# Performance work log

Hardware: AMD Instinct MI355X
Metric: run time of the kernel (lower is better)

Reference implementation:

```python
import jax, jax.numpy as jnp
import numpy as np

NTYPES = 2
NATOMS = (512, 512)
N = 1024          # total atoms
NN = 128          # neighbors per type
M = NTYPES * NN   # 256 neighbor slots per atom
D = 25            # last embedding width
FH = 240          # fitting hidden width
B = 8
RMIN, RMAX = 5.8, 6.0


def _embed_mlp(s, W0, b0, W1, b1, W2, b2):
    # DeepMD-style resnet embedding net: 1 -> D -> D -> D, tanh + skip
    h = jnp.tanh(s @ W0 + b0)
    h = h + jnp.tanh(h @ W1 + b1)
    h = h + jnp.tanh(h @ W2 + b2)
    return h


def setup_inputs() -> dict:
    key = jax.random.key(0)
    ks = jax.random.split(key, 20)
    # relative positions; components in [-4.5, 4.5] so |r| spans <5.8, [5.8,6.0), >=6.0
    image_dR = (jax.random.uniform(ks[0], (B, N, NTYPES, NN, 3), jnp.float32) - 0.5) * 9.0
    # 0 == empty neighbor slot (mask = list_neigh > 0); index-1 in [0, N)
    list_neigh = jax.random.randint(ks[1], (B, N, NTYPES, NN), 0, 1025)
    davg = 0.1 * jax.random.normal(ks[2], (NTYPES, M, 4), jnp.float32)
    dstd = jax.random.uniform(ks[3], (NTYPES, M, 4), jnp.float32, 0.5, 1.5)
    P = NTYPES * NTYPES
    eW0 = jax.random.normal(ks[4], (P, 1, D), jnp.float32)
    eb0 = 0.1 * jax.random.normal(ks[5], (P, D), jnp.float32)
    eW1 = jax.random.normal(ks[6], (P, D, D), jnp.float32) / np.sqrt(D)
    eb1 = 0.1 * jax.random.normal(ks[7], (P, D), jnp.float32)
    eW2 = jax.random.normal(ks[8], (P, D, D), jnp.float32) / np.sqrt(D)
    eb2 = 0.1 * jax.random.normal(ks[9], (P, D), jnp.float32)
    fW0 = jax.random.normal(ks[10], (NTYPES, 16 * D, FH), jnp.float32) / np.sqrt(16 * D)
    fb0 = 0.1 * jax.random.normal(ks[11], (NTYPES, FH), jnp.float32)
    fW1 = jax.random.normal(ks[12], (NTYPES, FH, FH), jnp.float32) / np.sqrt(FH)
    fb1 = 0.1 * jax.random.normal(ks[13], (NTYPES, FH), jnp.float32)
    fW2 = jax.random.normal(ks[14], (NTYPES, FH, FH), jnp.float32) / np.sqrt(FH)
    fb2 = 0.1 * jax.random.normal(ks[15], (NTYPES, FH), jnp.float32)
    fW3 = jax.random.normal(ks[16], (NTYPES, FH, 1), jnp.float32) / np.sqrt(FH)
    fb3 = 0.1 * jax.random.normal(ks[17], (NTYPES, 1), jnp.float32)
    ener_shift = 0.01 * jax.random.normal(ks[18], (NTYPES,), jnp.float32)
    return {
        'image_dR': image_dR, 'list_neigh': list_neigh,
        'davg': davg, 'dstd': dstd,
        'eW0': eW0, 'eb0': eb0, 'eW1': eW1, 'eb1': eb1, 'eW2': eW2, 'eb2': eb2,
        'fW0': fW0, 'fb0': fb0, 'fW1': fW1, 'fb1': fb1, 'fW2': fW2, 'fb2': fb2,
        'fW3': fW3, 'fb3': fb3, 'ener_shift': ener_shift,
        'dfeat': jnp.zeros((1,), jnp.float32),
        'Egroup_weight': jnp.zeros((1,), jnp.float32),
        'divider': jnp.ones((1,), jnp.float32),
    }


def _forward(image_dR, list_neigh, davg, dstd,
             eW0, eb0, eW1, eb1, eW2, eb2,
             fW0, fb0, fW1, fb1, fW2, fb2, fW3, fb3, ener_shift):
    dR = image_dR.reshape(B, N, M, 3)
    neigh = list_neigh.reshape(B, N, M)
    mask = neigh > 0
    mf = mask.astype(dR.dtype)
    dR2 = jnp.sum(dR * dR, axis=-1)                       # [B,N,M]
    safe_dR2 = jnp.where(mask, dR2, 1.0)
    Rij = jnp.sqrt(safe_dR2)
    inr = mf / Rij                                        # 1/|r|, 0 off-mask
    x = Rij * mf                                          # nr = dR2/Rij = |r|
    Ri_xyz = dR / safe_dR2[..., None] * mf[..., None]     # r / |r|^2
    inr2 = inr * inr
    inr4 = inr2 * inr2
    inr3 = inr4 * x
    # smooth switching function on [RMIN, RMAX]
    u = (x - RMIN) / (RMAX - RMIN)
    poly = u * u * u * (-6.0 * u * u + 15.0 * u - 10.0) + 1.0
    dpoly = (3.0 * u * u * (-6.0 * u * u + 15.0 * u - 10.0)
             + u * u * u * (-12.0 * u + 15.0)) / (RMAX - RMIN)
    mid = (x >= RMIN) & (x < RMAX)
    vv = jnp.where(x < RMIN, 1.0, jnp.where(mid, poly, 0.0)) * mf
    dvv = jnp.where(mid, dpoly, 0.0) * mf
    Ri_pre = jnp.concatenate([inr[..., None], Ri_xyz], axis=-1)   # [B,N,M,4]
    common = (dvv * inr)[..., None] * dR                          # [B,N,M,3]
    row0 = dR * (inr3 * vv)[..., None] - Ri_pre[..., 0:1] * common
    eye = jnp.eye(3, dtype=dR.dtype)
    outer = (2.0 * dR[..., :, None] * dR[..., None, :] * inr4[..., None, None]
             - eye * inr2[..., None, None])                       # [B,N,M,3,3]
    rows = outer * vv[..., None, None] - Ri_pre[..., 1:4, None] * common[..., None, :]
    Ri_d = jnp.concatenate([row0[..., None, :], rows], axis=-2) * mf[..., None, None]  # [B,N,M,4,3]
    Ri = Ri_pre * vv[..., None]
    # per-type normalization stats broadcast over atoms of each type
    davg_res = jnp.concatenate([jnp.broadcast_to(davg[t], (NATOMS[t], M, 4)) for t in range(NTYPES)], axis=0)
    dstd_res = jnp.concatenate([jnp.broadcast_to(dstd[t], (NATOMS[t], M, 4)) for t in range(NTYPES)], axis=0)
    Ri = (Ri - davg_res) / dstd_res
    Ri_d = Ri_d / dstd_res[..., None]

    def ei_fn(Ri_n):
        Ei_list = []
        start = 0
        for t in range(NTYPES):
            na = NATOMS[t]
            Rt = jax.lax.slice_in_dim(Ri_n, start, start + na, axis=1)  # [B,na,M,4]
            acc = jnp.zeros((B, na, 4, D), Ri_n.dtype)
            for t1 in range(NTYPES):
                p = t * NTYPES + t1
                blk = Rt[:, :, t1 * NN:(t1 + 1) * NN]                  # [B,na,NN,4]
                G = _embed_mlp(blk[..., 0:1], eW0[p], eb0[p], eW1[p], eb1[p], eW2[p], eb2[p])
                acc = acc + jnp.einsum('bnkd,bnke->bnde', blk, G)
            acc = acc * (4.0 / (NN * NTYPES * 4))
            DRt = jnp.einsum('bnde,bndf->bnef', acc, acc[..., :16]).reshape(B, na, D * 16)
            h = jnp.tanh(DRt @ fW0[t] + fb0[t])
            h = h + jnp.tanh(h @ fW1[t] + fb1[t])
            h = h + jnp.tanh(h @ fW2[t] + fb2[t])
            Ei_list.append(h @ fW3[t] + fb3[t] + ener_shift[t])
            start += na
        return jnp.concatenate(Ei_list, axis=1)   # [B,N,1]

    Ei, vjpf = jax.vjp(ei_fn, Ri)
    dE, = vjpf(jnp.ones_like(Ei))                 # dEi/dRi  [B,N,M,4]
    Etot = jnp.sum(Ei, axis=1)                    # [B,1]
    pair = jnp.einsum('bnmd,bnmdx->bnmx', dE, Ri_d)   # per-pair force term [B,N,M,3]
    F_self = -jnp.sum(pair, axis=2)
    j = neigh - 1
    valid = j >= 0
    flat_idx = jnp.where(valid, j, N) + jnp.arange(B)[:, None, None] * (N + 1)
    contrib = jnp.where(valid[..., None], pair, 0.0)
    seg = jax.ops.segment_sum(contrib.reshape(-1, 3), flat_idx.reshape(-1), num_segments=B * (N + 1))
    F = F_self + seg.reshape(B, N + 1, 3)[:, :N]
    return Etot, Ei, F


def reference(image_dR, list_neigh, davg, dstd,
              eW0, eb0, eW1, eb1, eW2, eb2,
              fW0, fb0, fW1, fb1, fW2, fb2, fW3, fb3, ener_shift,
              dfeat, Egroup_weight, divider):
    # dfeat / Egroup_weight / divider are in the torch forward signature but unused
    return _forward(image_dR, list_neigh, davg, dstd,
                    eW0, eb0, eW1, eb1, eW2, eb2,
                    fW0, fb0, fW1, fb1, fW2, fb2, fW3, fb3, ener_shift)
```

## Files before the change

### kernel.cpp

```cpp
#include <hip/hip_runtime.h>

#define DEV __device__ __forceinline__

namespace {

constexpr int B_ = 8;
constexpr int N_ = 1024;
constexpr int M_ = 256;
constexpr int D_ = 25;
constexpr int FH_ = 240;
constexpr int NATOM = B_ * N_;
constexpr float CSC = 1.0f / 256.0f;

DEV float fast_tanh(float x) {
  float ax = fabsf(x);
  float e = __expf(-2.0f * ax);
  float r = (1.0f - e) * __builtin_amdgcn_rcpf(1.0f + e);
  return copysignf(r, x);
}

template <bool WANT_RID>
DEV void compute_geom(float dx, float dy, float dz, int nb, int t, int m,
                      const float* __restrict__ davg, const float* __restrict__ dstd,
                      float* __restrict__ blk, float* __restrict__ rid) {
  float mf = (nb > 0) ? 1.0f : 0.0f;
  float dr2 = dx * dx + dy * dy + dz * dz;
  float safe = (nb > 0) ? dr2 : 1.0f;
  float rs = __builtin_amdgcn_rsqf(safe);
  float rij = safe * rs;
  float inr = mf * rs;
  float x = rij * mf;
  float inr2 = inr * inr;
  float inr4 = inr2 * inr2;
  float inr3 = inr4 * x;
  float u = (x - 5.8f) * 5.0f;
  float uu = u * u;
  float A = -6.0f * uu + 15.0f * u - 10.0f;
  float poly = uu * u * A + 1.0f;
  float dpoly = (3.0f * uu * A + uu * u * (-12.0f * u + 15.0f)) * 5.0f;
  bool mid = (x >= 5.8f) && (x < 6.0f);
  float vv = ((x < 5.8f) ? 1.0f : (mid ? poly : 0.0f)) * mf;
  float dvv = (mid ? dpoly : 0.0f) * mf;
  float pre[4];
  pre[0] = inr;
  pre[1] = dx * inr2;
  pre[2] = dy * inr2;
  pre[3] = dz * inr2;
  int bidx = (t * M_ + m) * 4;
  float4 av = *(const float4*)(davg + bidx);
  float4 sv = *(const float4*)(dstd + bidx);
  float avf[4] = {av.x, av.y, av.z, av.w};
  float rsv[4] = {__builtin_amdgcn_rcpf(sv.x), __builtin_amdgcn_rcpf(sv.y),
                  __builtin_amdgcn_rcpf(sv.z), __builtin_amdgcn_rcpf(sv.w)};
#pragma unroll
  for (int d = 0; d < 4; ++d) blk[d] = (pre[d] * vv - avf[d]) * rsv[d];
  if (WANT_RID) {
    float dv[3] = {dx, dy, dz};
    float ci = dvv * inr;
    float com[3];
#pragma unroll
    for (int c = 0; c < 3; ++c) com[c] = ci * dv[c];
    float iv = inr3 * vv;
#pragma unroll
    for (int c = 0; c < 3; ++c)
      rid[c] = (dv[c] * iv - pre[0] * com[c]) * mf * rsv[0];
#pragma unroll
    for (int r = 0; r < 3; ++r) {
#pragma unroll
      for (int c = 0; c < 3; ++c) {
        float outer = 2.0f * dv[r] * dv[c] * inr4 - ((r == c) ? inr2 : 0.0f);
        rid[(1 + r) * 3 + c] = (outer * vv - pre[1 + r] * com[c]) * mf * rsv[1 + r];
      }
    }
  }
}

DEV void embed_fwd(float s, const float* __restrict__ W0, const float* __restrict__ b0,
                   const float* __restrict__ W1, const float* __restrict__ b1,
                   const float* __restrict__ W2, const float* __restrict__ b2,
                   float* __restrict__ h0, float* __restrict__ t1v,
                   float* __restrict__ h1, float* __restrict__ t2v) {
#pragma unroll
  for (int e = 0; e < D_; ++e) h0[e] = fast_tanh(fmaf(s, W0[e], b0[e]));
  float a[D_];
#pragma unroll
  for (int e = 0; e < D_; ++e) a[e] = b1[e];
#pragma unroll
  for (int f = 0; f < D_; ++f) {
    float hf = h0[f];
#pragma unroll
    for (int e = 0; e < D_; ++e) a[e] = fmaf(hf, W1[f * D_ + e], a[e]);
  }
#pragma unroll
  for (int e = 0; e < D_; ++e) { t1v[e] = fast_tanh(a[e]); h1[e] = h0[e] + t1v[e]; }
#pragma unroll
  for (int e = 0; e < D_; ++e) a[e] = b2[e];
#pragma unroll
  for (int f = 0; f < D_; ++f) {
    float hf = h1[f];
#pragma unroll
    for (int e = 0; e < D_; ++e) a[e] = fmaf(hf, W2[f * D_ + e], a[e]);
  }
#pragma unroll
  for (int e = 0; e < D_; ++e) t2v[e] = fast_tanh(a[e]);
}

__global__ __launch_bounds__(256, 2) void k_embed_acc(
    const float* __restrict__ dR, const int* __restrict__ neigh,
    const float* __restrict__ davg, const float* __restrict__ dstd,
    const float* __restrict__ eW0, const float* __restrict__ eb0,
    const float* __restrict__ eW1, const float* __restrict__ eb1,
    const float* __restrict__ eW2, const float* __restrict__ eb2,
    float* __restrict__ acc_ws) {
  __shared__ float sG[M_ * D_];
  __shared__ float4 sBlk[M_];
  int atom = blockIdx.x;
  int n = atom & (N_ - 1);
  int t = (n >= 512) ? 1 : 0;
  int m = threadIdx.x;
  int p = __builtin_amdgcn_readfirstlane(t * 2 + (m >> 7));
  const float* W0 = eW0 + p * D_;
  const float* b0 = eb0 + p * D_;
  const float* W1 = eW1 + p * D_ * D_;
  const float* b1 = eb1 + p * D_;
  const float* W2 = eW2 + p * D_ * D_;
  const float* b2 = eb2 + p * D_;
  int base = atom * M_ + m;
  float dx = dR[base * 3 + 0];
  float dy = dR[base * 3 + 1];
  float dz = dR[base * 3 + 2];
  int nb = neigh[base];
  float blk[4];
  compute_geom<false>(dx, dy, dz, nb, t, m, davg, dstd, blk, nullptr);
  float h0[D_], t1v[D_], h1[D_], t2v[D_];
  embed_fwd(blk[0], W0, b0, W1, b1, W2, b2, h0, t1v, h1, t2v);
#pragma unroll
  for (int e = 0; e < D_; ++e) sG[m * D_ + e] = h1[e] + t2v[e];
  sBlk[m] = make_float4(blk[0], blk[1], blk[2], blk[3]);
  __syncthreads();
  if (threadIdx.x < 100) {
    int d = threadIdx.x & 3;
    int e = threadIdx.x >> 2;
    const float* sb = (const float*)sBlk;
    float sum = 0.0f;
    for (int mm = 0; mm < M_; ++mm)
      sum = fmaf(sb[mm * 4 + d], sG[mm * D_ + e], sum);
    acc_ws[atom * 100 + d * D_ + e] = sum * CSC;
  }
}

__global__ __launch_bounds__(256) void k_fit(
    const float* __restrict__ acc_ws,
    const float* __restrict__ fW0, const float* __restrict__ fb0,
    const float* __restrict__ fW1, const float* __restrict__ fb1,
    const float* __restrict__ fW2, const float* __restrict__ fb2,
    const float* __restrict__ fW3, const float* __restrict__ fb3,
    const float* __restrict__ ener_shift,
    float* __restrict__ dacc_ws, float* __restrict__ out) {
  constexpr int AB = 8;
  __shared__ float sAcc[AB][100];
  __shared__ float sX[AB][400];
  __shared__ float sH0[AB][FH_];
  __shared__ float sT1[AB][FH_];
  __shared__ float sH1[AB][FH_];
  __shared__ float sT2[AB][FH_];
  __shared__ float sEi[AB];
  int a0 = blockIdx.x * AB;
  int bb = a0 >> 10;
  int n0 = a0 & (N_ - 1);
  int t = (n0 >= 512) ? 1 : 0;
  int tid = threadIdx.x;
  for (int idx = tid; idx < AB * 100; idx += 256)
    ((float*)sAcc)[idx] = acc_ws[a0 * 100 + idx];
  if (tid < AB) sEi[tid] = 0.0f;
  __syncthreads();
  for (int idx = tid; idx < AB * 400; idx += 256) {
    int a = idx / 400; int r = idx % 400; int e = r >> 4; int f = r & 15;
    const float* A = sAcc[a];
    sX[a][r] = A[e] * A[f] + A[25 + e] * A[25 + f] + A[50 + e] * A[50 + f] +
               A[75 + e] * A[75 + f];
  }
  __syncthreads();
  const float* W0 = fW0 + t * 400 * FH_;
  const float* W1 = fW1 + t * FH_ * FH_;
  const float* W2 = fW2 + t * FH_ * FH_;
  const float* B0 = fb0 + t * FH_;
  const float* B1 = fb1 + t * FH_;
  const float* B2 = fb2 + t * FH_;
  const float* W3 = fW3 + t * FH_;
  int j = tid;
  if (j < FH_) {
    float acc8[AB];
#pragma unroll
    for (int a = 0; a < AB; ++a) acc8[a] = B0[j];
    for (int i = 0; i < 400; ++i) {
      float w = W0[i * FH_ + j];
#pragma unroll
      for (int a = 0; a < AB; ++a) acc8[a] = fmaf(sX[a][i], w, acc8[a]);
    }
#pragma unroll
    for (int a = 0; a < AB; ++a) sH0[a][j] = fast_tanh(acc8[a]);
  }
  __syncthreads();
  if (j < FH_) {
    float acc8[AB];
#pragma unroll
    for (int a = 0; a < AB; ++a) acc8[a] = B1[j];
    for (int f = 0; f < FH_; ++f) {
      float w = W1[f * FH_ + j];
#pragma unroll
      for (int a = 0; a < AB; ++a) acc8[a] = fmaf(sH0[a][f], w, acc8[a]);
    }
#pragma unroll
    for (int a = 0; a < AB; ++a) {
      float tv = fast_tanh(acc8[a]);
      sT1[a][j] = tv;
      sH1[a][j] = sH0[a][j] + tv;
    }
  }
  __syncthreads();
  if (j < FH_) {
    float acc8[AB];
#pragma unroll
    for (int a = 0; a < AB; ++a) acc8[a] = B2[j];
    for (int f = 0; f < FH_; ++f) {
      float w = W2[f * FH_ + j];
#pragma unroll
      for (int a = 0; a < AB; ++a) acc8[a] = fmaf(sH1[a][f], w, acc8[a]);
    }
    float w3 = W3[j];
#pragma unroll
    for (int a = 0; a < AB; ++a) {
      float tv = fast_tanh(acc8[a]);
      sT2[a][j] = tv;
      atomicAdd(&sEi[a], (sH1[a][j] + tv) * w3);
    }
  }
  __syncthreads();
  if (tid < AB) {
    float ei = sEi[tid] + fb3[t] + ener_shift[t];
    out[8 + a0 + tid] = ei;
    atomicAdd(&out[bb], ei);
  }
  if (j < FH_) {
    float w3 = W3[j];
#pragma unroll
    for (int a = 0; a < AB; ++a) {
      float tv = sT2[a][j];
      sT2[a][j] = w3 * (1.0f - tv * tv);
    }
  }
  __syncthreads();
  if (j < FH_) {
    float w3 = W3[j];
    float acc8[AB];
#pragma unroll
    for (int a = 0; a < AB; ++a) acc8[a] = w3;
    for (int k = 0; k < FH_; ++k) {
      float w = W2[j * FH_ + k];
#pragma unroll
      for (int a = 0; a < AB; ++a) acc8[a] = fmaf(sT2[a][k], w, acc8[a]);
    }
#pragma unroll
    for (int a = 0; a < AB; ++a) {
      float dh1 = acc8[a];
      float tv = sT1[a][j];
      sH1[a][j] = dh1;
      sT1[a][j] = dh1 * (1.0f - tv * tv);
    }
  }
  __syncthreads();
  if (j < FH_) {
    float acc8[AB];
#pragma unroll
    for (int a = 0; a < AB; ++a) acc8[a] = sH1[a][j];
    for (int k = 0; k < FH_; ++k) {
      float w = W1[j * FH_ + k];
#pragma unroll
      for (int a = 0; a < AB; ++a) acc8[a] = fmaf(sT1[a][k], w, acc8[a]);
    }
#pragma unroll
    for (int a = 0; a < AB; ++a) {
      float h0v = sH0[a][j];
      sH0[a][j] = acc8[a] * (1.0f - h0v * h0v);
    }
  }
  __syncthreads();
  for (int i = tid; i < 400; i += 256) {
    float acc8[AB];
#pragma unroll
    for (int a = 0; a < AB; ++a) acc8[a] = 0.0f;
    for (int jj = 0; jj < FH_; ++jj) {
      float w = W0[i * FH_ + jj];
#pragma unroll
      for (int a = 0; a < AB; ++a) acc8[a] = fmaf(sH0[a][jj], w, acc8[a]);
    }
#pragma unroll
    for (int a = 0; a < AB; ++a) sX[a][i] = acc8[a];
  }
  __syncthreads();
  for (int idx = tid; idx < AB * 100; idx += 256) {
    int a = idx / 100; int r = idx % 100; int d = r / 25; int e = r % 25;
    const float* A = sAcc[a];
    const float* DX = sX[a];
    float sum = 0.0f;
#pragma unroll
    for (int f = 0; f < 16; ++f) sum = fmaf(DX[e * 16 + f], A[d * 25 + f], sum);
    if (e < 16) {
#pragma unroll
      for (int e2 = 0; e2 < 25; ++e2) sum = fmaf(DX[e2 * 16 + e], A[d * 25 + e2], sum);
    }
    dacc_ws[a0 * 100 + idx] = sum;
  }
}

__global__ __launch_bounds__(256, 2) void k_bwd_force(
    const float* __restrict__ dR, const int* __restrict__ neigh,
    const float* __restrict__ davg, const float* __restrict__ dstd,
    const float* __restrict__ eW0, const float* __restrict__ eb0,
    const float* __restrict__ eW1, const float* __restrict__ eb1,
    const float* __restrict__ eW2, const float* __restrict__ eb2,
    const float* __restrict__ dacc_ws, float* __restrict__ out) {
  __shared__ float sF[3];
  int atom = blockIdx.x;
  int bb = atom >> 10;
  int n = atom & (N_ - 1);
  int t = (n >= 512) ? 1 : 0;
  int m = threadIdx.x;
  if (m < 3) sF[m] = 0.0f;
  __syncthreads();
  int p = __builtin_amdgcn_readfirstlane(t * 2 + (m >> 7));
  const float* W0 = eW0 + p * D_;
  const float* b0 = eb0 + p * D_;
  const float* W1 = eW1 + p * D_ * D_;
  const float* b1 = eb1 + p * D_;
  const float* W2 = eW2 + p * D_ * D_;
  const float* b2 = eb2 + p * D_;
  const float* dac = dacc_ws + atom * 100;
  int base = atom * M_ + m;
  float dx = dR[base * 3 + 0];
  float dy = dR[base * 3 + 1];
  float dz = dR[base * 3 + 2];
  int nb = neigh[base];
  float blk[4], rid[12];
  compute_geom<true>(dx, dy, dz, nb, t, m, davg, dstd, blk, rid);
  float h0[D_], t1v[D_], h1[D_], t2v[D_];
  embed_fwd(blk[0], W0, b0, W1, b1, W2, b2, h0, t1v, h1, t2v);
  float dblk[4];
#pragma unroll
  for (int d = 0; d < 4; ++d) {
    float s = 0.0f;
#pragma unroll
    for (int e = 0; e < D_; ++e) s = fmaf(dac[d * D_ + e], h1[e] + t2v[e], s);
    dblk[d] = s * CSC;
  }
  float dG[D_];
#pragma unroll
  for (int e = 0; e < D_; ++e)
    dG[e] = CSC * (dac[e] * blk[0] + dac[25 + e] * blk[1] +
                   dac[50 + e] * blk[2] + dac[75 + e] * blk[3]);
  float g[D_];
#pragma unroll
  for (int e = 0; e < D_; ++e) g[e] = dG[e] * (1.0f - t2v[e] * t2v[e]);
#pragma unroll
  for (int e = 0; e < D_; ++e) {
    float s = dG[e];
#pragma unroll
    for (int f = 0; f < D_; ++f) s = fmaf(g[f], W2[e * D_ + f], s);
    dG[e] = s;
  }
#pragma unroll
  for (int e = 0; e < D_; ++e) g[e] = dG[e] * (1.0f - t1v[e] * t1v[e]);
#pragma unroll
  for (int e = 0; e < D_; ++e) {
    float s = dG[e];
#pragma unroll
    for (int f = 0; f < D_; ++f) s = fmaf(g[f], W1[e * D_ + f], s);
    dG[e] = s;
  }
  float ds = 0.0f;
#pragma unroll
  for (int e = 0; e < D_; ++e) ds = fmaf(dG[e] * (1.0f - h0[e] * h0[e]), W0[e], ds);
  float dE0 = dblk[0] + ds, dE1 = dblk[1], dE2 = dblk[2], dE3 = dblk[3];
  float px = dE0 * rid[0] + dE1 * rid[3] + dE2 * rid[6] + dE3 * rid[9];
  float py = dE0 * rid[1] + dE1 * rid[4] + dE2 * rid[7] + dE3 * rid[10];
  float pz = dE0 * rid[2] + dE1 * rid[5] + dE2 * rid[8] + dE3 * rid[11];
  atomicAdd(&sF[0], px);
  atomicAdd(&sF[1], py);
  atomicAdd(&sF[2], pz);
  if (nb > 0) {
    int jn = nb - 1;
    int fi = 8 + NATOM + (bb * N_ + jn) * 3;
    atomicAdd(&out[fi + 0], px);
    atomicAdd(&out[fi + 1], py);
    atomicAdd(&out[fi + 2], pz);
  }
  __syncthreads();
  if (m < 3) atomicAdd(&out[8 + NATOM + atom * 3 + m], -sF[m]);
}

}

extern "C" void kernel_launch(void* const* d_in, const int* in_sizes, int n_in,
                              void* d_out, int out_size, void* d_ws, size_t ws_size,
                              hipStream_t stream) {
  (void)in_sizes; (void)n_in; (void)ws_size;
  const float* image_dR   = (const float*)d_in[0];
  const int*   list_neigh = (const int*)d_in[1];
  const float* davg       = (const float*)d_in[2];
  const float* dstd       = (const float*)d_in[3];
  const float* eW0        = (const float*)d_in[4];
  const float* eb0        = (const float*)d_in[5];
  const float* eW1        = (const float*)d_in[6];
  const float* eb1        = (const float*)d_in[7];
  const float* eW2        = (const float*)d_in[8];
  const float* eb2        = (const float*)d_in[9];
  const float* fW0        = (const float*)d_in[10];
  const float* fb0        = (const float*)d_in[11];
  const float* fW1        = (const float*)d_in[12];
  const float* fb1        = (const float*)d_in[13];
  const float* fW2        = (const float*)d_in[14];
  const float* fb2        = (const float*)d_in[15];
  const float* fW3        = (const float*)d_in[16];
  const float* fb3        = (const float*)d_in[17];
  const float* ener_shift = (const float*)d_in[18];
  float* out = (float*)d_out;
  float* acc_ws  = (float*)d_ws;
  float* dacc_ws = acc_ws + NATOM * 100;

  hipMemsetAsync(d_out, 0, (size_t)out_size * sizeof(float), stream);
  k_embed_acc<<<NATOM, 256, 0, stream>>>(image_dR, list_neigh, davg, dstd,
                                         eW0, eb0, eW1, eb1, eW2, eb2, acc_ws);
  k_fit<<<NATOM / 8, 256, 0, stream>>>(acc_ws, fW0, fb0, fW1, fb1, fW2, fb2,
                                       fW3, fb3, ener_shift, dacc_ws, out);
  k_bwd_force<<<NATOM, 256, 0, stream>>>(image_dR, list_neigh, davg, dstd,
                                         eW0, eb0, eW1, eb1, eW2, eb2,
                                         dacc_ws, out);
}
```

Before: 1.054 ms.

## Hand-unroll embedding nets into scalars and restructure reductions across all kernels

Replaces the array-based embedding forward and backward code with macro-expanded scalar variables so everything stays in registers. Raises k_embed_acc and k_fit occupancy hints to 4 blocks per SM and transposes the shared G/blk tiles so the contraction reads float4 vectors. The backward kernel splits geometry into a block pass and a force pass that folds dE into the rid terms directly, and it reduces per-atom self forces with wave shuffles before the shared atomics. k_fit now sums the per-atom energies in shared memory before issuing one global atomic. Higher occupancy hints may force register spills.

```diff
diff --git a/kernel.cpp b/kernel.cpp
--- a/kernel.cpp
+++ b/kernel.cpp
@@ -1,6 +1,13 @@
 #include <hip/hip_runtime.h>
 
 #define DEV __device__ __forceinline__
+
+#define RA(F) F(0) F(1) F(2) F(3) F(4) F(5) F(6) F(7) F(8) F(9) F(10) F(11) \
+  F(12) F(13) F(14) F(15) F(16) F(17) F(18) F(19) F(20) F(21) F(22) F(23) F(24)
+#define RB(F,j) F(j,0) F(j,1) F(j,2) F(j,3) F(j,4) F(j,5) F(j,6) F(j,7) F(j,8) \
+  F(j,9) F(j,10) F(j,11) F(j,12) F(j,13) F(j,14) F(j,15) F(j,16) F(j,17) \
+  F(j,18) F(j,19) F(j,20) F(j,21) F(j,22) F(j,23) F(j,24)
+#define AP8(F) F(0) F(1) F(2) F(3) F(4) F(5) F(6) F(7)
 
 namespace {
 
@@ -19,10 +26,36 @@
   return copysignf(r, x);
 }
 
-template <bool WANT_RID>
-DEV void compute_geom(float dx, float dy, float dz, int nb, int t, int m,
-                      const float* __restrict__ davg, const float* __restrict__ dstd,
-                      float* __restrict__ blk, float* __restrict__ rid) {
+DEV void geom_blk(float dx, float dy, float dz, int nb, int t, int m,
+                  const float* __restrict__ davg, const float* __restrict__ dstd,
+                  float& o0, float& o1, float& o2, float& o3) {
+  float mf = (nb > 0) ? 1.0f : 0.0f;
+  float dr2 = dx * dx + dy * dy + dz * dz;
+  float safe = (nb > 0) ? dr2 : 1.0f;
+  float rs = __builtin_amdgcn_rsqf(safe);
+  float rij = safe * rs;
+  float inr = mf * rs;
+  float x = rij * mf;
+  float inr2 = inr * inr;
+  float u = (x - 5.8f) * 5.0f;
+  float uu = u * u;
+  float A = -6.0f * uu + 15.0f * u - 10.0f;
+  float poly = uu * u * A + 1.0f;
+  bool mid = (x >= 5.8f) && (x < 6.0f);
+  float vv = ((x < 5.8f) ? 1.0f : (mid ? poly : 0.0f)) * mf;
+  int bidx = (t * M_ + m) * 4;
+  float4 av = *(const float4*)(davg + bidx);
+  float4 sv = *(const float4*)(dstd + bidx);
+  o0 = (inr * vv - av.x) * __builtin_amdgcn_rcpf(sv.x);
+  o1 = (dx * inr2 * vv - av.y) * __builtin_amdgcn_rcpf(sv.y);
+  o2 = (dy * inr2 * vv - av.z) * __builtin_amdgcn_rcpf(sv.z);
+  o3 = (dz * inr2 * vv - av.w) * __builtin_amdgcn_rcpf(sv.w);
+}
+
+DEV void geom_force(float dx, float dy, float dz, int nb, int t, int m,
+                    const float* __restrict__ dstd,
+                    float dE0, float dE1, float dE2, float dE3,
+                    float& px, float& py, float& pz) {
   float mf = (nb > 0) ? 1.0f : 0.0f;
   float dr2 = dx * dx + dy * dy + dz * dz;
   float safe = (nb > 0) ? dr2 : 1.0f;
@@ -41,115 +74,108 @@
   bool mid = (x >= 5.8f) && (x < 6.0f);
   float vv = ((x < 5.8f) ? 1.0f : (mid ? poly : 0.0f)) * mf;
   float dvv = (mid ? dpoly : 0.0f) * mf;
-  float pre[4];
-  pre[0] = inr;
-  pre[1] = dx * inr2;
-  pre[2] = dy * inr2;
-  pre[3] = dz * inr2;
   int bidx = (t * M_ + m) * 4;
-  float4 av = *(const float4*)(davg + bidx);
   float4 sv = *(const float4*)(dstd + bidx);
-  float avf[4] = {av.x, av.y, av.z, av.w};
-  float rsv[4] = {__builtin_amdgcn_rcpf(sv.x), __builtin_amdgcn_rcpf(sv.y),
-                  __builtin_amdgcn_rcpf(sv.z), __builtin_amdgcn_rcpf(sv.w)};
-#pragma unroll
-  for (int d = 0; d < 4; ++d) blk[d] = (pre[d] * vv - avf[d]) * rsv[d];
-  if (WANT_RID) {
-    float dv[3] = {dx, dy, dz};
-    float ci = dvv * inr;
-    float com[3];
-#pragma unroll
-    for (int c = 0; c < 3; ++c) com[c] = ci * dv[c];
-    float iv = inr3 * vv;
-#pragma unroll
-    for (int c = 0; c < 3; ++c)
-      rid[c] = (dv[c] * iv - pre[0] * com[c]) * mf * rsv[0];
-#pragma unroll
-    for (int r = 0; r < 3; ++r) {
-#pragma unroll
-      for (int c = 0; c < 3; ++c) {
-        float outer = 2.0f * dv[r] * dv[c] * inr4 - ((r == c) ? inr2 : 0.0f);
-        rid[(1 + r) * 3 + c] = (outer * vv - pre[1 + r] * com[c]) * mf * rsv[1 + r];
-      }
-    }
-  }
-}
-
-DEV void embed_fwd(float s, const float* __restrict__ W0, const float* __restrict__ b0,
-                   const float* __restrict__ W1, const float* __restrict__ b1,
-                   const float* __restrict__ W2, const float* __restrict__ b2,
-                   float* __restrict__ h0, float* __restrict__ t1v,
-                   float* __restrict__ h1, float* __restrict__ t2v) {
-#pragma unroll
-  for (int e = 0; e < D_; ++e) h0[e] = fast_tanh(fmaf(s, W0[e], b0[e]));
-  float a[D_];
-#pragma unroll
-  for (int e = 0; e < D_; ++e) a[e] = b1[e];
-#pragma unroll
-  for (int f = 0; f < D_; ++f) {
-    float hf = h0[f];
-#pragma unroll
-    for (int e = 0; e < D_; ++e) a[e] = fmaf(hf, W1[f * D_ + e], a[e]);
-  }
-#pragma unroll
-  for (int e = 0; e < D_; ++e) { t1v[e] = fast_tanh(a[e]); h1[e] = h0[e] + t1v[e]; }
-#pragma unroll
-  for (int e = 0; e < D_; ++e) a[e] = b2[e];
-#pragma unroll
-  for (int f = 0; f < D_; ++f) {
-    float hf = h1[f];
-#pragma unroll
-    for (int e = 0; e < D_; ++e) a[e] = fmaf(hf, W2[f * D_ + e], a[e]);
-  }
-#pragma unroll
-  for (int e = 0; e < D_; ++e) t2v[e] = fast_tanh(a[e]);
-}
-
-__global__ __launch_bounds__(256, 2) void k_embed_acc(
+  float e0 = dE0 * mf * __builtin_amdgcn_rcpf(sv.x);
+  float e1 = dE1 * mf * __builtin_amdgcn_rcpf(sv.y);
+  float e2 = dE2 * mf * __builtin_amdgcn_rcpf(sv.z);
+  float e3 = dE3 * mf * __builtin_amdgcn_rcpf(sv.w);
+  float ci = dvv * inr;
+  float comx = ci * dx, comy = ci * dy, comz = ci * dz;
+  float iv = inr3 * vv;
+  float pre0 = inr, pre1 = dx * inr2, pre2 = dy * inr2, pre3 = dz * inr2;
+  float txx = 2.0f * dx * dx * inr4 - inr2;
+  float tyy = 2.0f * dy * dy * inr4 - inr2;
+  float tzz = 2.0f * dz * dz * inr4 - inr2;
+  float txy = 2.0f * dx * dy * inr4;
+  float txz = 2.0f * dx * dz * inr4;
+  float tyz = 2.0f * dy * dz * inr4;
+  px = e0 * (dx * iv - pre0 * comx) + e1 * (txx * vv - pre1 * comx) +
+       e2 * (txy * vv - pre2 * comx) + e3 * (txz * vv - pre3 * comx);
+  py = e0 * (dy * iv - pre0 * comy) + e1 * (txy * vv - pre1 * comy) +
+       e2 * (tyy * vv - pre2 * comy) + e3 * (tyz * vv - pre3 * comy);
+  pz = e0 * (dz * iv - pre0 * comz) + e1 * (txz * vv - pre1 * comz) +
+       e2 * (tyz * vv - pre2 * comz) + e3 * (tzz * vv - pre3 * comz);
+}
+
+#define K1H0(e) float h##e = fast_tanh(fmaf(s0, W0p[e], b0p[e]));
+#define K1A1(e) float a##e = b1p[e];
+#define K1M1E(f,e) a##e = fmaf(hf, W1p[(f)*25+(e)], a##e);
+#define K1M1R(f) { const float hf = h##f; RB(K1M1E, f) }
+#define K1H1(e) h##e += fast_tanh(a##e);
+#define K1A2(e) a##e = b2p[e];
+#define K1M2E(f,e) a##e = fmaf(hf, W2p[(f)*25+(e)], a##e);
+#define K1M2R(f) { const float hf = h##f; RB(K1M2E, f) }
+#define K1ST(e) sGT[e][m] = h##e + fast_tanh(a##e);
+
+__global__ __launch_bounds__(256, 4) void k_embed_acc(
     const float* __restrict__ dR, const int* __restrict__ neigh,
     const float* __restrict__ davg, const float* __restrict__ dstd,
     const float* __restrict__ eW0, const float* __restrict__ eb0,
     const float* __restrict__ eW1, const float* __restrict__ eb1,
     const float* __restrict__ eW2, const float* __restrict__ eb2,
     float* __restrict__ acc_ws) {
-  __shared__ float sG[M_ * D_];
-  __shared__ float4 sBlk[M_];
+  __shared__ float sGT[D_][260];
+  __shared__ float sBT[4][260];
   int atom = blockIdx.x;
   int n = atom & (N_ - 1);
   int t = (n >= 512) ? 1 : 0;
   int m = threadIdx.x;
   int p = __builtin_amdgcn_readfirstlane(t * 2 + (m >> 7));
-  const float* W0 = eW0 + p * D_;
-  const float* b0 = eb0 + p * D_;
-  const float* W1 = eW1 + p * D_ * D_;
-  const float* b1 = eb1 + p * D_;
-  const float* W2 = eW2 + p * D_ * D_;
-  const float* b2 = eb2 + p * D_;
+  const float* W0p = eW0 + p * D_;
+  const float* b0p = eb0 + p * D_;
+  const float* W1p = eW1 + p * 625;
+  const float* b1p = eb1 + p * D_;
+  const float* W2p = eW2 + p * 625;
+  const float* b2p = eb2 + p * D_;
   int base = atom * M_ + m;
   float dx = dR[base * 3 + 0];
   float dy = dR[base * 3 + 1];
   float dz = dR[base * 3 + 2];
   int nb = neigh[base];
-  float blk[4];
-  compute_geom<false>(dx, dy, dz, nb, t, m, davg, dstd, blk, nullptr);
-  float h0[D_], t1v[D_], h1[D_], t2v[D_];
-  embed_fwd(blk[0], W0, b0, W1, b1, W2, b2, h0, t1v, h1, t2v);
-#pragma unroll
-  for (int e = 0; e < D_; ++e) sG[m * D_ + e] = h1[e] + t2v[e];
-  sBlk[m] = make_float4(blk[0], blk[1], blk[2], blk[3]);
+  float bb0, bb1, bb2, bb3;
+  geom_blk(dx, dy, dz, nb, t, m, davg, dstd, bb0, bb1, bb2, bb3);
+  float s0 = bb0;
+  RA(K1H0)
+  RA(K1A1)
+  RA(K1M1R)
+  RA(K1H1)
+  RA(K1A2)
+  RA(K1M2R)
+  RA(K1ST)
+  sBT[0][m] = bb0; sBT[1][m] = bb1; sBT[2][m] = bb2; sBT[3][m] = bb3;
   __syncthreads();
   if (threadIdx.x < 100) {
+    int e = threadIdx.x >> 2;
     int d = threadIdx.x & 3;
-    int e = threadIdx.x >> 2;
-    const float* sb = (const float*)sBlk;
+    const float4* g4 = (const float4*)(&sGT[e][0]);
+    const float4* b4 = (const float4*)(&sBT[d][0]);
     float sum = 0.0f;
-    for (int mm = 0; mm < M_; ++mm)
-      sum = fmaf(sb[mm * 4 + d], sG[mm * D_ + e], sum);
+    for (int k = 0; k < 64; ++k) {
+      float4 g = g4[k];
+      float4 b = b4[k];
+      sum += b.x * g.x + b.y * g.y + b.z * g.z + b.w * g.w;
+    }
     acc_ws[atom * 100 + d * D_ + e] = sum * CSC;
   }
 }
 
-__global__ __launch_bounds__(256) void k_fit(
+#define DECL8(v) float c0=(v),c1=(v),c2=(v),c3=(v),c4=(v),c5=(v),c6=(v),c7=(v);
+#define F8X(q)  c##q = fmaf(sX[q][i], w, c##q);
+#define F8H0(q) c##q = fmaf(sH0[q][f], w, c##q);
+#define F8H1(q) c##q = fmaf(sH1[q][f], w, c##q);
+#define F8T2(q) c##q = fmaf(sT2[q][k], w, c##q);
+#define F8T1(q) c##q = fmaf(sT1[q][k], w, c##q);
+#define F8G0(q) c##q = fmaf(sH0[q][jj], w, c##q);
+#define L0S(q) sH0[q][j] = fast_tanh(c##q);
+#define L1S(q) { float tv = fast_tanh(c##q); sT1[q][j] = tv; sH1[q][j] = sH0[q][j] + tv; }
+#define L2S(q) { float tv = fast_tanh(c##q); sT2[q][j] = tv; atomicAdd(&sEi[q], (sH1[q][j] + tv) * w3); }
+#define G2S(q) { float tv = sT2[q][j]; sT2[q][j] = w3 * (1.0f - tv * tv); }
+#define D1S(q) { float dh1 = c##q; float tv = sT1[q][j]; sH1[q][j] = dh1; sT1[q][j] = dh1 * (1.0f - tv * tv); }
+#define D0S(q) { float h0v = sH0[q][j]; sH0[q][j] = c##q * (1.0f - h0v * h0v); }
+#define DXS(q) sX[q][i] = c##q;
+
+__global__ __launch_bounds__(256, 4) void k_fit(
     const float* __restrict__ acc_ws,
     const float* __restrict__ fW0, const float* __restrict__ fb0,
     const float* __restrict__ fW1, const float* __restrict__ fb1,
@@ -190,113 +216,56 @@
   const float* W3 = fW3 + t * FH_;
   int j = tid;
   if (j < FH_) {
-    float acc8[AB];
-#pragma unroll
-    for (int a = 0; a < AB; ++a) acc8[a] = B0[j];
-    for (int i = 0; i < 400; ++i) {
-      float w = W0[i * FH_ + j];
-#pragma unroll
-      for (int a = 0; a < AB; ++a) acc8[a] = fmaf(sX[a][i], w, acc8[a]);
-    }
-#pragma unroll
-    for (int a = 0; a < AB; ++a) sH0[a][j] = fast_tanh(acc8[a]);
-  }
-  __syncthreads();
-  if (j < FH_) {
-    float acc8[AB];
-#pragma unroll
-    for (int a = 0; a < AB; ++a) acc8[a] = B1[j];
-    for (int f = 0; f < FH_; ++f) {
-      float w = W1[f * FH_ + j];
-#pragma unroll
-      for (int a = 0; a < AB; ++a) acc8[a] = fmaf(sH0[a][f], w, acc8[a]);
-    }
-#pragma unroll
-    for (int a = 0; a < AB; ++a) {
-      float tv = fast_tanh(acc8[a]);
-      sT1[a][j] = tv;
-      sH1[a][j] = sH0[a][j] + tv;
-    }
-  }
-  __syncthreads();
-  if (j < FH_) {
-    float acc8[AB];
-#pragma unroll
-    for (int a = 0; a < AB; ++a) acc8[a] = B2[j];
-    for (int f = 0; f < FH_; ++f) {
-      float w = W2[f * FH_ + j];
-#pragma unroll
-      for (int a = 0; a < AB; ++a) acc8[a] = fmaf(sH1[a][f], w, acc8[a]);
-    }
+    DECL8(B0[j])
+    for (int i = 0; i < 400; ++i) { float w = W0[i * FH_ + j]; AP8(F8X) }
+    AP8(L0S)
+  }
+  __syncthreads();
+  if (j < FH_) {
+    DECL8(B1[j])
+    for (int f = 0; f < FH_; ++f) { float w = W1[f * FH_ + j]; AP8(F8H0) }
+    AP8(L1S)
+  }
+  __syncthreads();
+  if (j < FH_) {
+    DECL8(B2[j])
+    for (int f = 0; f < FH_; ++f) { float w = W2[f * FH_ + j]; AP8(F8H1) }
     float w3 = W3[j];
-#pragma unroll
-    for (int a = 0; a < AB; ++a) {
-      float tv = fast_tanh(acc8[a]);
-      sT2[a][j] = tv;
-      atomicAdd(&sEi[a], (sH1[a][j] + tv) * w3);
-    }
+    AP8(L2S)
   }
   __syncthreads();
   if (tid < AB) {
     float ei = sEi[tid] + fb3[t] + ener_shift[t];
     out[8 + a0 + tid] = ei;
-    atomicAdd(&out[bb], ei);
+    sEi[tid] = ei;
   }
   if (j < FH_) {
     float w3 = W3[j];
-#pragma unroll
-    for (int a = 0; a < AB; ++a) {
-      float tv = sT2[a][j];
-      sT2[a][j] = w3 * (1.0f - tv * tv);
-    }
-  }
-  __syncthreads();
-  if (j < FH_) {
-    float w3 = W3[j];
-    float acc8[AB];
-#pragma unroll
-    for (int a = 0; a < AB; ++a) acc8[a] = w3;
-    for (int k = 0; k < FH_; ++k) {
-      float w = W2[j * FH_ + k];
-#pragma unroll
-      for (int a = 0; a < AB; ++a) acc8[a] = fmaf(sT2[a][k], w, acc8[a]);
-    }
-#pragma unroll
-    for (int a = 0; a < AB; ++a) {
-      float dh1 = acc8[a];
-      float tv = sT1[a][j];
-      sH1[a][j] = dh1;
-      sT1[a][j] = dh1 * (1.0f - tv * tv);
-    }
-  }
-  __syncthreads();
-  if (j < FH_) {
-    float acc8[AB];
-#pragma unroll
-    for (int a = 0; a < AB; ++a) acc8[a] = sH1[a][j];
-    for (int k = 0; k < FH_; ++k) {
-      float w = W1[j * FH_ + k];
-#pragma unroll
-      for (int a = 0; a < AB; ++a) acc8[a] = fmaf(sT1[a][k], w, acc8[a]);
-    }
-#pragma unroll
-    for (int a = 0; a < AB; ++a) {
-      float h0v = sH0[a][j];
-      sH0[a][j] = acc8[a] * (1.0f - h0v * h0v);
-    }
+    AP8(G2S)
+  }
+  __syncthreads();
+  if (tid == 0) {
+    float s = sEi[0] + sEi[1] + sEi[2] + sEi[3] + sEi[4] + sEi[5] + sEi[6] + sEi[7];
+    atomicAdd(&out[bb], s);
+  }
+  if (j < FH_) {
+    DECL8(W3[j])
+    for (int k = 0; k < FH_; ++k) { float w = W2[j * FH_ + k]; AP8(F8T2) }
+    AP8(D1S)
+  }
+  __syncthreads();
+  if (j < FH_) {
+    DECL8(sH1[0][j])
+    c1 = sH1[1][j]; c2 = sH1[2][j]; c3 = sH1[3][j];
+    c4 = sH1[4][j]; c5 = sH1[5][j]; c6 = sH1[6][j]; c7 = sH1[7][j];
+    for (int k = 0; k < FH_; ++k) { float w = W1[j * FH_ + k]; AP8(F8T1) }
+    AP8(D0S)
   }
   __syncthreads();
   for (int i = tid; i < 400; i += 256) {
-    float acc8[AB];
-#pragma unroll
-    for (int a = 0; a < AB; ++a) acc8[a] = 0.0f;
-    for (int jj = 0; jj < FH_; ++jj) {
-      float w = W0[i * FH_ + jj];
-#pragma unroll
-      for (int a = 0; a < AB; ++a) acc8[a] = fmaf(sH0[a][jj], w, acc8[a]);
-    }
-#pragma unroll
-    for (int a = 0; a < AB; ++a) sX[a][i] = acc8[a];
+    DECL8(0.0f)
+    for (int jj = 0; jj < FH_; ++jj) { float w = W0[i * FH_ + jj]; AP8(F8G0) }
+    AP8(DXS)
   }
   __syncthreads();
   for (int idx = tid; idx < AB * 100; idx += 256) {
@@ -313,6 +282,28 @@
     dacc_ws[a0 * 100 + idx] = sum;
   }
 }
+
+#define K3H0(e) float x##e = fast_tanh(fmaf(s0, W0p[e], b0p[e]));
+#define K3A1(e) float a##e = b1p[e];
+#define K3M1E(f,e) a##e = fmaf(hf, W1p[(f)*25+(e)], a##e);
+#define K3M1R(f) { const float hf = x##f; RB(K3M1E, f) }
+#define K3T1(e) float t##e = fast_tanh(a##e); x##e += t##e;
+#define K3A2(e) a##e = b2p[e];
+#define K3M2E(f,e) a##e = fmaf(hf, W2p[(f)*25+(e)], a##e);
+#define K3M2R(f) { const float hf = x##f; RB(K3M2E, f) }
+#define K3DY(e) float y##e;
+#define K3SD(e) { float t2 = fast_tanh(a##e); float G = x##e + t2; \
+  db0 = fmaf(dacp[e], G, db0); db1 = fmaf(dacp[25+(e)], G, db1); \
+  db2 = fmaf(dacp[50+(e)], G, db2); db3 = fmaf(dacp[75+(e)], G, db3); \
+  float dg = CSC * (dacp[e] * bb0 + dacp[25+(e)] * bb1 + \
+                    dacp[50+(e)] * bb2 + dacp[75+(e)] * bb3); \
+  y##e = dg * (1.0f - t2 * t2); a##e = dg; }
+#define K3SEF(e,f) s = fmaf(y##f, W2p[(e)*25+(f)], s);
+#define K3SE(e) { float s = a##e; RB(K3SEF, e) a##e = s; }
+#define K3G1(e) y##e = a##e * (1.0f - t##e * t##e);
+#define K3SFF(e,f) s = fmaf(y##f, W1p[(e)*25+(f)], s);
+#define K3SF(e) { float s = a##e; RB(K3SFF, e) float h0e = x##e - t##e; \
+  dsum = fmaf(s * (1.0f - h0e * h0e), W0p[e], dsum); }
 
 __global__ __launch_bounds__(256, 2) void k_bwd_force(
     const float* __restrict__ dR, const int* __restrict__ neigh,
@@ -330,64 +321,52 @@
   if (m < 3) sF[m] = 0.0f;
   __syncthreads();
   int p = __builtin_amdgcn_readfirstlane(t * 2 + (m >> 7));
-  const float* W0 = eW0 + p * D_;
-  const float* b0 = eb0 + p * D_;
-  const float* W1 = eW1 + p * D_ * D_;
-  const float* b1 = eb1 + p * D_;
-  const float* W2 = eW2 + p * D_ * D_;
-  const float* b2 = eb2 + p * D_;
-  const float* dac = dacc_ws + atom * 100;
+  const float* W0p = eW0 + p * D_;
+  const float* b0p = eb0 + p * D_;
+  const float* W1p = eW1 + p * 625;
+  const float* b1p = eb1 + p * D_;
+  const float* W2p = eW2 + p * 625;
+  const float* b2p = eb2 + p * D_;
+  const float* dacp = dacc_ws + atom * 100;
   int base = atom * M_ + m;
   float dx = dR[base * 3 + 0];
   float dy = dR[base * 3 + 1];
   float dz = dR[base * 3 + 2];
   int nb = neigh[base];
-  float blk[4], rid[12];
-  compute_geom<true>(dx, dy, dz, nb, t, m, davg, dstd, blk, rid);
-  float h0[D_], t1v[D_], h1[D_], t2v[D_];
-  embed_fwd(blk[0], W0, b0, W1, b1, W2, b2, h0, t1v, h1, t2v);
-  float dblk[4];
+  float bb0, bb1, bb2, bb3;
+  geom_blk(dx, dy, dz, nb, t, m, davg, dstd, bb0, bb1, bb2, bb3);
+  float s0 = bb0;
+  RA(K3H0)
+  RA(K3A1)
+  RA(K3M1R)
+  RA(K3T1)
+  RA(K3A2)
+  RA(K3M2R)
+  RA(K3DY)
+  float db0 = 0.0f, db1 = 0.0f, db2 = 0.0f, db3 = 0.0f;
+  RA(K3SD)
+  RA(K3SE)
+  RA(K3G1)
+  float dsum = 0.0f;
+  RA(K3SF)
+  float dE0 = db0 * CSC + dsum;
+  float dE1 = db1 * CSC;
+  float dE2 = db2 * CSC;
+  float dE3 = db3 * CSC;
+  float px, py, pz;
+  geom_force(dx, dy, dz, nb, t, m, dstd, dE0, dE1, dE2, dE3, px, py, pz);
+  float rx = px, ry = py, rz = pz;
 #pragma unroll
-  for (int d = 0; d < 4; ++d) {
-    float s = 0.0f;
-#pragma unroll
-    for (int e = 0; e < D_; ++e) s = fmaf(dac[d * D_ + e], h1[e] + t2v[e], s);
-    dblk[d] = s * CSC;
-  }
-  float dG[D_];
-#pragma unroll
-  for (int e = 0; e < D_; ++e)
-    dG[e] = CSC * (dac[e] * blk[0] + dac[25 + e] * blk[1] +
-                   dac[50 + e] * blk[2] + dac[75 + e] * blk[3]);
-  float g[D_];
-#pragma unroll
-  for (int e = 0; e < D_; ++e) g[e] = dG[e] * (1.0f - t2v[e] * t2v[e]);
-#pragma unroll
-  for (int e = 0; e < D_; ++e) {
-    float s = dG[e];
-#pragma unroll
-    for (int f = 0; f < D_; ++f) s = fmaf(g[f], W2[e * D_ + f], s);
-    dG[e] = s;
-  }
-#pragma unroll
-  for (int e = 0; e < D_; ++e) g[e] = dG[e] * (1.0f - t1v[e] * t1v[e]);
-#pragma unroll
-  for (int e = 0; e < D_; ++e) {
-    float s = dG[e];
-#pragma unroll
-    for (int f = 0; f < D_; ++f) s = fmaf(g[f], W1[e * D_ + f], s);
-    dG[e] = s;
-  }
-  float ds = 0.0f;
-#pragma unroll
-  for (int e = 0; e < D_; ++e) ds = fmaf(dG[e] * (1.0f - h0[e] * h0[e]), W0[e], ds);
-  float dE0 = dblk[0] + ds, dE1 = dblk[1], dE2 = dblk[2], dE3 = dblk[3];
-  float px = dE0 * rid[0] + dE1 * rid[3] + dE2 * rid[6] + dE3 * rid[9];
-  float py = dE0 * rid[1] + dE1 * rid[4] + dE2 * rid[7] + dE3 * rid[10];
-  float pz = dE0 * rid[2] + dE1 * rid[5] + dE2 * rid[8] + dE3 * rid[11];
-  atomicAdd(&sF[0], px);
-  atomicAdd(&sF[1], py);
-  atomicAdd(&sF[2], pz);
+  for (int off = 32; off > 0; off >>= 1) {
+    rx += __shfl_down(rx, off, 64);
+    ry += __shfl_down(ry, off, 64);
+    rz += __shfl_down(rz, off, 64);
+  }
+  if ((m & 63) == 0) {
+    atomicAdd(&sF[0], rx);
+    atomicAdd(&sF[1], ry);
+    atomicAdd(&sF[2], rz);
+  }
   if (nb > 0) {
     int jn = nb - 1;
     int fi = 8 + NATOM + (bb * N_ + jn) * 3;
```

Result: slower. 1.150 ms (+9.2%).
